# Kernel tuning notes

Hardware: AMD Instinct MI355X
Metric: run time of the kernel (lower is better)

## Reference

```python
import jax, jax.numpy as jnp
import numpy as np

H, D, BS = 32, 128, 16  # num heads, head dim, paged-KV block size
ROPE_BASE = 10000.0
NEG_INF = -1e30


def setup_inputs() -> dict:
    key = jax.random.key(0)
    ks = jax.random.split(key, 8)
    B, KV, hidden = 8, 2048, H * D  # decode: one new token per sequence
    max_blocks = KV // BS
    num_slots = B * KV

    hidden_states = jax.random.normal(ks[0], (B, hidden), jnp.float32) * 0.02

    # rotary cos/sin for the current position of each sequence (pos = KV-1)
    inv_freq = 1.0 / (ROPE_BASE ** (jnp.arange(0, D, 2, dtype=jnp.float32) / D))
    pos = jnp.full((B,), KV - 1, jnp.float32)
    ang = pos[:, None] * inv_freq[None, :]            # [B, D/2]
    cos, sin = jnp.cos(ang), jnp.sin(ang)

    w_qkv = jax.random.normal(ks[1], (3 * H * D, hidden), jnp.float32) * 0.02
    b_qkv = jax.random.normal(ks[2], (3 * H * D,), jnp.float32) * 0.02
    w_o = jax.random.normal(ks[3], (hidden, H * D), jnp.float32) * 0.02

    k_cache = jax.random.normal(ks[4], (num_slots, H, D), jnp.float32) * 0.5
    v_cache = jax.random.normal(ks[5], (num_slots, H, D), jnp.float32) * 0.5

    # contiguous block allocation: seq b owns blocks [b*max_blocks, (b+1)*max_blocks)
    block_tables = jnp.arange(B * max_blocks, dtype=jnp.int32).reshape(B, max_blocks)
    slots = (jnp.arange(B, dtype=jnp.int32) * KV + (KV - 1)).astype(jnp.int32)
    input_lengths = jnp.full((B,), KV, jnp.int32)

    return dict(hidden_states=hidden_states, cos=cos, sin=sin,
                w_qkv=w_qkv, b_qkv=b_qkv, w_o=w_o,
                k_cache=k_cache, v_cache=v_cache,
                block_tables=block_tables, slots=slots,
                input_lengths=input_lengths, max_s=KV)


def _rope(x, cos, sin):
    # flash-attn style (non-interleaved) rotary: split head dim in halves
    x1, x2 = jnp.split(x, 2, axis=-1)                 # [T, H, D/2] each
    c, s = cos[:, None, :], sin[:, None, :]
    return jnp.concatenate([x1 * c - x2 * s, x1 * s + x2 * c], axis=-1)


def reference(hidden_states, cos, sin, w_qkv, b_qkv, w_o,
              k_cache, v_cache, block_tables, slots, input_lengths, max_s):
    B = hidden_states.shape[0]
    # fused QKV projection (c_attn, bias=True)
    qkv = hidden_states @ w_qkv.T + b_qkv             # [B, 3*H*D]
    q, k, v = jnp.split(qkv, 3, axis=1)
    q = q.reshape(B, H, D)
    k = k.reshape(B, H, D)
    v = v.reshape(B, H, D)

    # rotary applied in-place to q and k[:,0] in the original
    q = _rope(q, cos, sin)
    k = _rope(k, cos, sin)

    # reshape_and_cache: scatter current k/v into the paged KV cache
    k_cache = k_cache.at[slots].set(k)
    v_cache = v_cache.at[slots].set(v)

    # paged_attn: gather KV via block tables, masked softmax over valid length
    pos = jnp.arange(max_s)                           # [S]
    idx = block_tables[:, pos // BS] * BS + (pos % BS)[None, :]  # [B, S] slot ids
    keys = k_cache[idx]                               # [B, S, H, D]
    vals = v_cache[idx]                               # [B, S, H, D]

    scale = D ** -0.5
    scores = jnp.einsum('bhd,bshd->bhs', q, keys) * scale
    valid = pos[None, :] < input_lengths[:, None]     # [B, S]
    scores = jnp.where(valid[:, None, :], scores, NEG_INF)
    probs = jax.nn.softmax(scores, axis=-1)
    attn = jnp.einsum('bhs,bshd->bhd', probs, vals)   # [B, H, D]

    # o_proj (c_proj, bias=False)
    return attn.reshape(B, H * D) @ w_o.T
```

## Files before the change

kernel.cpp:

```cpp
#include <hip/hip_runtime.h>

#define NH 32
#define HD 128
#define PBS 16
#define HIDDEN (NH * HD)
#define QKVN (3 * HIDDEN)
#define NSPLIT 4

__global__ __launch_bounds__(256) void gemv8(const float* __restrict__ x,
                                             const float* __restrict__ W,
                                             const float* __restrict__ bias,
                                             float* __restrict__ out,
                                             int N, int K) {
    const int lane = threadIdx.x & 63;
    const int gw   = (blockIdx.x * blockDim.x + threadIdx.x) >> 6;
    const int nwv  = (gridDim.x * blockDim.x) >> 6;
    for (int n = gw; n < N; n += nwv) {
        const float* wrow = W + (size_t)n * K;
        float acc[8];
#pragma unroll
        for (int b = 0; b < 8; ++b) acc[b] = 0.f;
#pragma unroll 4
        for (int k0 = lane * 4; k0 < K; k0 += 256) {
            const float4 w4 = *reinterpret_cast<const float4*>(wrow + k0);
#pragma unroll
            for (int b = 0; b < 8; ++b) {
                const float4 x4 = *reinterpret_cast<const float4*>(x + (size_t)b * K + k0);
                acc[b] += w4.x * x4.x + w4.y * x4.y + w4.z * x4.z + w4.w * x4.w;
            }
        }
#pragma unroll
        for (int b = 0; b < 8; ++b) {
#pragma unroll
            for (int off = 32; off > 0; off >>= 1)
                acc[b] += __shfl_xor(acc[b], off, 64);
        }
        if (lane == 0) {
            const float bv = bias ? bias[n] : 0.f;
#pragma unroll
            for (int b = 0; b < 8; ++b)
                out[(size_t)b * N + n] = acc[b] + bv;
        }
    }
}

__global__ __launch_bounds__(256) void rope_k(float* __restrict__ qkv,
                                              const float* __restrict__ cosb,
                                              const float* __restrict__ sinb,
                                              int B) {
    const int tid = blockIdx.x * blockDim.x + threadIdx.x;
    const int total = 2 * B * NH * (HD / 2);
    if (tid >= total) return;
    const int d = tid % (HD / 2);
    const int h = (tid / (HD / 2)) % NH;
    const int b = (tid / (HD / 2) / NH) % B;
    const int part = tid / (HD / 2) / NH / B;
    const float c = cosb[b * (HD / 2) + d];
    const float s = sinb[b * (HD / 2) + d];
    float* p = qkv + (size_t)b * QKVN + part * HIDDEN + h * HD + d;
    const float x1 = p[0];
    const float x2 = p[HD / 2];
    p[0]      = x1 * c - x2 * s;
    p[HD / 2] = x1 * s + x2 * c;
}

__global__ __launch_bounds__(512) void attn_part(const float* __restrict__ qkv,
                                                 const float* __restrict__ k_cache,
                                                 const float* __restrict__ v_cache,
                                                 const int* __restrict__ block_tables,
                                                 const int* __restrict__ slots,
                                                 const int* __restrict__ lengths,
                                                 float* __restrict__ part_o,
                                                 float* __restrict__ part_ml,
                                                 int S, int max_blocks) {
    const int split = blockIdx.x & (NSPLIT - 1);
    const int bh    = blockIdx.x >> 2;
    const int b     = bh >> 5;
    const int h     = bh & 31;
    const int SP    = S / NSPLIT;
    const int base  = split * SP;

    extern __shared__ float smem[];
    float* sc    = smem;
    int*   bt    = (int*)(smem + SP);
    float* red   = smem + SP + SP / PBS;
    float* stage = red + 16;

    const int tid  = threadIdx.x;
    const int lane = tid & 63;
    const int wid  = tid >> 6;
    const int nw   = blockDim.x >> 6;
    const int half = lane >> 5;
    const int l32  = lane & 31;

    const int nbt = SP / PBS;
    for (int i = tid; i < nbt; i += blockDim.x)
        bt[i] = block_tables[b * max_blocks + base / PBS + i];
    __syncthreads();

    const int slot_b = slots[b];
    const int len    = lengths[b];
    const float scale = 0.088388347648318447f;

    const float* qp   = qkv + (size_t)b * QKVN + h * HD;
    const float* newk = qkv + (size_t)b * QKVN + HIDDEN + h * HD;
    const float* newv = qkv + (size_t)b * QKVN + 2 * HIDDEN + h * HD;
    const float4 q4 = *reinterpret_cast<const float4*>(qp + l32 * 4);

    const int STEP = nw * 16;
    for (int s0 = wid * 16; s0 < SP; s0 += STEP) {
        float4 k4[8];
#pragma unroll
        for (int u = 0; u < 8; ++u) {
            const int p = s0 + u * 2 + half;
            const int idx = bt[p >> 4] * PBS + (p & (PBS - 1));
            const float* kp = (idx == slot_b) ? newk
                                              : (k_cache + (size_t)idx * HIDDEN + h * HD);
            k4[u] = *reinterpret_cast<const float4*>(kp + l32 * 4);
        }
#pragma unroll
        for (int u = 0; u < 8; ++u) {
            const int p = s0 + u * 2 + half;
            float d = k4[u].x * q4.x + k4[u].y * q4.y + k4[u].z * q4.z + k4[u].w * q4.w;
#pragma unroll
            for (int off = 16; off > 0; off >>= 1) d += __shfl_xor(d, off, 64);
            if (l32 == 0) sc[p] = (base + p < len) ? d * scale : -1e30f;
        }
    }
    __syncthreads();

    float m = -1e30f;
    for (int s = tid; s < SP; s += blockDim.x) m = fmaxf(m, sc[s]);
#pragma unroll
    for (int off = 32; off > 0; off >>= 1) m = fmaxf(m, __shfl_xor(m, off, 64));
    if (lane == 0) red[wid] = m;
    __syncthreads();
    float bm = red[0];
    for (int w = 1; w < nw; ++w) bm = fmaxf(bm, red[w]);
    __syncthreads();

    float lsum = 0.f;
    for (int s = tid; s < SP; s += blockDim.x) {
        const float e = __expf(sc[s] - bm);
        sc[s] = e;
        lsum += e;
    }
#pragma unroll
    for (int off = 32; off > 0; off >>= 1) lsum += __shfl_xor(lsum, off, 64);
    if (lane == 0) red[wid] = lsum;
    __syncthreads();
    float tot = 0.f;
    for (int w = 0; w < nw; ++w) tot += red[w];

    float4 acc[8];
#pragma unroll
    for (int u = 0; u < 8; ++u) acc[u] = make_float4(0.f, 0.f, 0.f, 0.f);
    for (int s0 = wid * 16; s0 < SP; s0 += STEP) {
        float4 v4[8];
        float pr[8];
#pragma unroll
        for (int u = 0; u < 8; ++u) {
            const int p = s0 + u * 2 + half;
            const int idx = bt[p >> 4] * PBS + (p & (PBS - 1));
            const float* vp = (idx == slot_b) ? newv
                                              : (v_cache + (size_t)idx * HIDDEN + h * HD);
            v4[u] = *reinterpret_cast<const float4*>(vp + l32 * 4);
            pr[u] = sc[p];
        }
#pragma unroll
        for (int u = 0; u < 8; ++u) {
            acc[u].x += pr[u] * v4[u].x;
            acc[u].y += pr[u] * v4[u].y;
            acc[u].z += pr[u] * v4[u].z;
            acc[u].w += pr[u] * v4[u].w;
        }
    }
    float4 a = acc[0];
#pragma unroll
    for (int u = 1; u < 8; ++u) {
        a.x += acc[u].x; a.y += acc[u].y; a.z += acc[u].z; a.w += acc[u].w;
    }
    a.x += __shfl_xor(a.x, 32, 64);
    a.y += __shfl_xor(a.y, 32, 64);
    a.z += __shfl_xor(a.z, 32, 64);
    a.w += __shfl_xor(a.w, 32, 64);

    if (half == 0)
        *reinterpret_cast<float4*>(&stage[wid * HD + l32 * 4]) = a;
    __syncthreads();
    if (wid == 0) {
        float t0 = 0.f, t1 = 0.f;
        for (int w = 0; w < nw; ++w) {
            t0 += stage[w * HD + lane * 2];
            t1 += stage[w * HD + lane * 2 + 1];
        }
        float* po = part_o + ((size_t)bh * NSPLIT + split) * HD;
        po[lane * 2]     = t0;
        po[lane * 2 + 1] = t1;
        if (lane == 0) {
            part_ml[((size_t)bh * NSPLIT + split) * 2]     = bm;
            part_ml[((size_t)bh * NSPLIT + split) * 2 + 1] = tot;
        }
    }
}

__global__ __launch_bounds__(HD) void attn_reduce(const float* __restrict__ part_o,
                                                  const float* __restrict__ part_ml,
                                                  float* __restrict__ attn_out) {
    const int bh = blockIdx.x;
    const int d  = threadIdx.x;
    float M = -1e30f;
#pragma unroll
    for (int i = 0; i < NSPLIT; ++i)
        M = fmaxf(M, part_ml[((size_t)bh * NSPLIT + i) * 2]);
    float L = 0.f, o = 0.f;
#pragma unroll
    for (int i = 0; i < NSPLIT; ++i) {
        const float mi = part_ml[((size_t)bh * NSPLIT + i) * 2];
        const float li = part_ml[((size_t)bh * NSPLIT + i) * 2 + 1];
        const float w  = __expf(mi - M);
        L += li * w;
        o += part_o[((size_t)bh * NSPLIT + i) * HD + d] * w;
    }
    attn_out[(size_t)bh * HD + d] = o / L;
}

extern "C" void kernel_launch(void* const* d_in, const int* in_sizes, int n_in,
                              void* d_out, int out_size, void* d_ws, size_t ws_size,
                              hipStream_t stream) {
    const float* hidden  = (const float*)d_in[0];
    const float* cosb    = (const float*)d_in[1];
    const float* sinb    = (const float*)d_in[2];
    const float* w_qkv   = (const float*)d_in[3];
    const float* b_qkv   = (const float*)d_in[4];
    const float* w_o     = (const float*)d_in[5];
    const float* k_cache = (const float*)d_in[6];
    const float* v_cache = (const float*)d_in[7];
    const int*   btab    = (const int*)d_in[8];
    const int*   slots   = (const int*)d_in[9];
    const int*   lens    = (const int*)d_in[10];

    const int B = in_sizes[0] / HIDDEN;
    const int max_blocks = in_sizes[8] / B;
    const int S = max_blocks * PBS;

    float* qkv     = (float*)d_ws;
    float* attn    = qkv + (size_t)B * QKVN;
    float* part_o  = attn + (size_t)B * HIDDEN;
    float* part_ml = part_o + (size_t)B * NH * NSPLIT * HD;
    float* out     = (float*)d_out;

    gemv8<<<QKVN / 4, 256, 0, stream>>>(hidden, w_qkv, b_qkv, qkv, QKVN, HIDDEN);

    {
        const int total = 2 * B * NH * (HD / 2);
        rope_k<<<(total + 255) / 256, 256, 0, stream>>>(qkv, cosb, sinb, B);
    }

    {
        const int SP = S / NSPLIT;
        const size_t smem = (size_t)(SP + SP / PBS + 16 + 8 * HD) * sizeof(float);
        attn_part<<<B * NH * NSPLIT, 512, smem, stream>>>(qkv, k_cache, v_cache,
                                                          btab, slots, lens,
                                                          part_o, part_ml, S, max_blocks);
        attn_reduce<<<B * NH, HD, 0, stream>>>(part_o, part_ml, attn);
    }

    gemv8<<<HIDDEN / 4, 256, 0, stream>>>(attn, w_o, nullptr, out, HIDDEN, HIDDEN);
}
```

Measured before the change: 211.8 us.

## Compute four weight rows per wavefront in GEMV and double attention KV splits

The GEMV kernel now has each wavefront handle four output rows at once. Each activation float4 load is reused across four weight rows instead of being reloaded per row, which cuts x reads and loop overhead. The attention partial kernel moves to 8 KV splits with 256-thread blocks, giving twice as many, smaller blocks for better occupancy. In exchange, register pressure rises from the 32 accumulators per lane, there are fewer GEMV waves, and the reduce kernel must merge twice as many partials.

```diff
diff --git a/kernel.cpp b/kernel.cpp
--- a/kernel.cpp
+++ b/kernel.cpp
@@ -5,41 +5,54 @@
 #define PBS 16
 #define HIDDEN (NH * HD)
 #define QKVN (3 * HIDDEN)
-#define NSPLIT 4
-
-__global__ __launch_bounds__(256) void gemv8(const float* __restrict__ x,
-                                             const float* __restrict__ W,
-                                             const float* __restrict__ bias,
-                                             float* __restrict__ out,
-                                             int N, int K) {
+#define NSPLIT 8
+
+__global__ __launch_bounds__(256) void gemv4r(const float* __restrict__ x,
+                                              const float* __restrict__ W,
+                                              const float* __restrict__ bias,
+                                              float* __restrict__ out,
+                                              int N, int K) {
     const int lane = threadIdx.x & 63;
-    const int gw   = (blockIdx.x * blockDim.x + threadIdx.x) >> 6;
-    const int nwv  = (gridDim.x * blockDim.x) >> 6;
-    for (int n = gw; n < N; n += nwv) {
-        const float* wrow = W + (size_t)n * K;
-        float acc[8];
-#pragma unroll
-        for (int b = 0; b < 8; ++b) acc[b] = 0.f;
-#pragma unroll 4
-        for (int k0 = lane * 4; k0 < K; k0 += 256) {
-            const float4 w4 = *reinterpret_cast<const float4*>(wrow + k0);
-#pragma unroll
-            for (int b = 0; b < 8; ++b) {
-                const float4 x4 = *reinterpret_cast<const float4*>(x + (size_t)b * K + k0);
-                acc[b] += w4.x * x4.x + w4.y * x4.y + w4.z * x4.z + w4.w * x4.w;
-            }
-        }
+    const int wv   = (blockIdx.x * blockDim.x + threadIdx.x) >> 6;
+    const int n0   = wv * 4;
+    if (n0 >= N) return;
+    const float* w0 = W + (size_t)n0 * K;
+
+    float acc[4][8];
+#pragma unroll
+    for (int r = 0; r < 4; ++r)
+#pragma unroll
+        for (int b = 0; b < 8; ++b) acc[r][b] = 0.f;
+
+#pragma unroll 2
+    for (int k0 = lane * 4; k0 < K; k0 += 256) {
+        float4 w4[4];
+#pragma unroll
+        for (int r = 0; r < 4; ++r)
+            w4[r] = *reinterpret_cast<const float4*>(w0 + (size_t)r * K + k0);
 #pragma unroll
         for (int b = 0; b < 8; ++b) {
+            const float4 x4 = *reinterpret_cast<const float4*>(x + (size_t)b * K + k0);
+#pragma unroll
+            for (int r = 0; r < 4; ++r)
+                acc[r][b] += w4[r].x * x4.x + w4[r].y * x4.y +
+                             w4[r].z * x4.z + w4[r].w * x4.w;
+        }
+    }
+#pragma unroll
+    for (int r = 0; r < 4; ++r)
+#pragma unroll
+        for (int b = 0; b < 8; ++b)
 #pragma unroll
             for (int off = 32; off > 0; off >>= 1)
-                acc[b] += __shfl_xor(acc[b], off, 64);
-        }
-        if (lane == 0) {
-            const float bv = bias ? bias[n] : 0.f;
+                acc[r][b] += __shfl_xor(acc[r][b], off, 64);
+    if (lane == 0) {
+#pragma unroll
+        for (int r = 0; r < 4; ++r) {
+            const float bv = bias ? bias[n0 + r] : 0.f;
 #pragma unroll
             for (int b = 0; b < 8; ++b)
-                out[(size_t)b * N + n] = acc[b] + bv;
+                out[(size_t)b * N + n0 + r] = acc[r][b] + bv;
         }
     }
 }
@@ -64,7 +77,7 @@
     p[HD / 2] = x1 * s + x2 * c;
 }
 
-__global__ __launch_bounds__(512) void attn_part(const float* __restrict__ qkv,
+__global__ __launch_bounds__(256) void attn_part(const float* __restrict__ qkv,
                                                  const float* __restrict__ k_cache,
                                                  const float* __restrict__ v_cache,
                                                  const int* __restrict__ block_tables,
@@ -73,8 +86,8 @@
                                                  float* __restrict__ part_o,
                                                  float* __restrict__ part_ml,
                                                  int S, int max_blocks) {
-    const int split = blockIdx.x & (NSPLIT - 1);
-    const int bh    = blockIdx.x >> 2;
+    const int split = blockIdx.x % NSPLIT;
+    const int bh    = blockIdx.x / NSPLIT;
     const int b     = bh >> 5;
     const int h     = bh & 31;
     const int SP    = S / NSPLIT;
@@ -250,7 +263,7 @@
     float* part_ml = part_o + (size_t)B * NH * NSPLIT * HD;
     float* out     = (float*)d_out;
 
-    gemv8<<<QKVN / 4, 256, 0, stream>>>(hidden, w_qkv, b_qkv, qkv, QKVN, HIDDEN);
+    gemv4r<<<QKVN / 16, 256, 0, stream>>>(hidden, w_qkv, b_qkv, qkv, QKVN, HIDDEN);
 
     {
         const int total = 2 * B * NH * (HD / 2);
@@ -259,12 +272,12 @@
 
     {
         const int SP = S / NSPLIT;
-        const size_t smem = (size_t)(SP + SP / PBS + 16 + 8 * HD) * sizeof(float);
-        attn_part<<<B * NH * NSPLIT, 512, smem, stream>>>(qkv, k_cache, v_cache,
+        const size_t smem = (size_t)(SP + SP / PBS + 16 + 4 * HD) * sizeof(float);
+        attn_part<<<B * NH * NSPLIT, 256, smem, stream>>>(qkv, k_cache, v_cache,
                                                           btab, slots, lens,
                                                           part_o, part_ml, S, max_blocks);
         attn_reduce<<<B * NH, HD, 0, stream>>>(part_o, part_ml, attn);
     }
 
-    gemv8<<<HIDDEN / 4, 256, 0, stream>>>(attn, w_o, nullptr, out, HIDDEN, HIDDEN);
-}
+    gemv4r<<<HIDDEN / 16, 256, 0, stream>>>(attn, w_o, nullptr, out, HIDDEN, HIDDEN);
+}
```

Result: faster. 205.7 us (-2.9%).
